# Kernel tuning notes

Hardware: AMD Instinct MI355X
Metric: run time of the kernel (lower is better)

## Reference

```python
import jax, jax.numpy as jnp
import numpy as np
import math

DIM = 1024
NUM_HEADS = 16
HEAD_DIM = DIM // NUM_HEADS
WINDOW = 256


def setup_inputs() -> dict:
    key = jax.random.key(0)
    k1, k2, k3 = jax.random.split(key, 3)
    B, T = 2, 2048
    x = jax.random.normal(k1, (B, T, DIM), dtype=jnp.float32)
    # nn.Linear weights: [out, in]; y = x @ W.T
    w_qkv = jax.random.normal(k2, (3 * DIM, DIM), dtype=jnp.float32) * (1.0 / math.sqrt(DIM))
    w_out = jax.random.normal(k3, (DIM, DIM), dtype=jnp.float32) * (1.0 / math.sqrt(DIM))
    return {"x": x, "w_qkv": w_qkv, "w_out": w_out}


def _apply_rotary(x, cos, sin):
    # x: [B,H,T,D]; cos/sin: [T, D//2] broadcast over B,H
    d = x.shape[-1] // 2
    x1, x2 = x[..., :d], x[..., d:]
    return jnp.concatenate([x1 * cos - x2 * sin, x2 * cos + x1 * sin], axis=-1)


def reference(x, w_qkv, w_out):
    B, T, C = x.shape
    H, Dh = NUM_HEADS, HEAD_DIM
    qkv = (x @ w_qkv.T).reshape(B, T, 3, H, Dh)
    q, k, v = qkv[:, :, 0], qkv[:, :, 1], qkv[:, :, 2]  # [B,T,H,Dh]
    q = jnp.transpose(q, (0, 2, 1, 3))  # [B,H,T,Dh]
    k = jnp.transpose(k, (0, 2, 1, 3))
    v = jnp.transpose(v, (0, 2, 1, 3))
    # RoPE tables
    inv_freq = 1.0 / (10000.0 ** (jnp.arange(0, Dh, 2, dtype=jnp.float32) / Dh))
    t = jnp.arange(T, dtype=jnp.float32)
    freqs = jnp.einsum('i,j->ij', t, inv_freq)  # [T, Dh//2]
    cos, sin = jnp.cos(freqs), jnp.sin(freqs)
    q = _apply_rotary(q, cos, sin)
    k = _apply_rotary(k, cos, sin)
    scale = 1.0 / math.sqrt(Dh)
    attn = jnp.einsum('bhqd,bhkd->bhqk', q, k) * scale  # [B,H,T,T]
    i = jnp.arange(T)[:, None]
    j = jnp.arange(T)[None, :]
    allowed = (j <= i) & ((i - j) < WINDOW)  # causal + sliding window
    attn = jnp.where(allowed, attn, -jnp.inf)
    attn = jax.nn.softmax(attn, axis=-1)
    out = jnp.einsum('bhqk,bhkd->bhqd', attn, v)
    out = jnp.transpose(out, (0, 2, 1, 3)).reshape(B, T, C)
    return out @ w_out.T
```

## Files before the change

kernel.cpp:

```cpp
#include <hip/hip_runtime.h>
#include <stdint.h>
#include <math.h>

#define T_SEQ 2048
#define NHEAD 16
#define WIN 256

typedef unsigned short u16;
typedef __attribute__((ext_vector_type(8))) short short8;
typedef __attribute__((ext_vector_type(4))) float f32x4;

typedef const __attribute__((address_space(1))) void* gas_ptr;
typedef __attribute__((address_space(3))) void* las_ptr;

__device__ __forceinline__ u16 f2bf(float f) {
  uint32_t u = __builtin_bit_cast(uint32_t, f);
  u += 0x7fffu + ((u >> 16) & 1u);
  return (u16)(u >> 16);
}
__device__ __forceinline__ float bf2f(u16 v) {
  return __builtin_bit_cast(float, ((uint32_t)v) << 16);
}
__device__ __forceinline__ void g2l16(const u16* g, u16* l) {
  __builtin_amdgcn_global_load_lds((gas_ptr)g, (las_ptr)l, 16, 0, 0);
}

__global__ __launch_bounds__(256) void cast_bf16_k(const float* __restrict__ in,
                                                   u16* __restrict__ out, int n4) {
  int i = blockIdx.x * 256 + threadIdx.x;
  if (i >= n4) return;
  const float4 v = reinterpret_cast<const float4*>(in)[i];
  union { u16 h[4]; uint64_t q; } o;
  o.h[0] = f2bf(v.x); o.h[1] = f2bf(v.y); o.h[2] = f2bf(v.z); o.h[3] = f2bf(v.w);
  reinterpret_cast<uint64_t*>(out)[i] = o.q;
}

template <typename OUT_T>
__global__ __launch_bounds__(256) void gemm_nt(const u16* __restrict__ A,
                                               const u16* __restrict__ B,
                                               OUT_T* __restrict__ C,
                                               int M, int N, int K) {
  __shared__ u16 lA[3][4096];
  __shared__ u16 lB[3][4096];
  const int tid = threadIdx.x;
  const int lane = tid & 63;
  const int wave = tid >> 6;
  const int r = lane & 15, g = lane >> 4;
  const int wr = wave >> 1, wc = wave & 1;

  const int nbn = N >> 7;
  const int bnpx = nbn >> 3;
  const int bid = blockIdx.x;
  const int xcd = bid & 7, ii = bid >> 3;
  const int bn = xcd * bnpx + (ii % bnpx);
  const int bm = ii / bnpx;

  const u16* Abase = A + (size_t)bm * 128 * K;
  const u16* Bbase = B + (size_t)bn * 128 * K;

  f32x4 acc[4][4];
#pragma unroll
  for (int m = 0; m < 4; m++)
#pragma unroll
    for (int n = 0; n < 4; n++) acc[m][n] = (f32x4){0.f, 0.f, 0.f, 0.f};

  const int c0 = tid, c1 = 256 + tid;
  const int row0 = c0 >> 2, row1 = c1 >> 2;
  const int sw0 = ((c0 & 3) ^ (row0 & 3)) * 8;
  const int sw1 = ((c1 & 3) ^ (row1 & 3)) * 8;
  const int ldsb = wave * 512;

  auto stage = [&](int k0, int b) {
    g2l16(Abase + (size_t)row0 * K + k0 + sw0, &lA[b][ldsb]);
    g2l16(Abase + (size_t)row1 * K + k0 + sw1, &lA[b][2048 + ldsb]);
    g2l16(Bbase + (size_t)row0 * K + k0 + sw0, &lB[b][ldsb]);
    g2l16(Bbase + (size_t)row1 * K + k0 + sw1, &lB[b][2048 + ldsb]);
  };

  const int nt = K >> 5;
  stage(0, 0);
  if (nt > 1) stage(32, 1);
  int cur = 0, pre = 2;

  const int rsw = (r & 3);
  for (int t = 0; t < nt; ++t) {
    if (t + 1 < nt) asm volatile("s_waitcnt vmcnt(4)" ::: "memory");
    else            asm volatile("s_waitcnt vmcnt(0)" ::: "memory");
    __builtin_amdgcn_s_barrier();
    if (t + 2 < nt) stage((t + 2) * 32, pre);

    const u16* la = lA[cur];
    const u16* lb = lB[cur];
    short8 af[4], bfr[4];
#pragma unroll
    for (int m = 0; m < 4; m++)
      af[m] = *reinterpret_cast<const short8*>(
          &la[(wr * 64 + m * 16 + r) * 32 + ((g ^ rsw) * 8)]);
#pragma unroll
    for (int n = 0; n < 4; n++)
      bfr[n] = *reinterpret_cast<const short8*>(
          &lb[(wc * 64 + n * 16 + r) * 32 + ((g ^ rsw) * 8)]);
#pragma unroll
    for (int m = 0; m < 4; m++)
#pragma unroll
      for (int n = 0; n < 4; n++)
        acc[m][n] = __builtin_amdgcn_mfma_f32_16x16x32_bf16(af[m], bfr[n], acc[m][n], 0, 0, 0);
    asm volatile("s_waitcnt lgkmcnt(0)" ::: "memory");
    cur = (cur == 2) ? 0 : cur + 1;
    pre = (pre == 2) ? 0 : pre + 1;
  }

#pragma unroll
  for (int m = 0; m < 4; m++) {
    const int row = bm * 128 + wr * 64 + m * 16 + g * 4;
#pragma unroll
    for (int n = 0; n < 4; n++) {
      const int col = bn * 128 + wc * 64 + n * 16 + r;
#pragma unroll
      for (int j = 0; j < 4; j++) {
        float v = acc[m][n][j];
        if constexpr (sizeof(OUT_T) == 2)
          C[(size_t)(row + j) * N + col] = f2bf(v);
        else
          C[(size_t)(row + j) * N + col] = v;
      }
    }
  }
}

__global__ __launch_bounds__(256) void rope_qk(const u16* __restrict__ qkv,
                                               u16* __restrict__ Qb,
                                               u16* __restrict__ Kb) {
  int idx = blockIdx.x * 256 + threadIdx.x;
  int d = idx & 31;
  int t = (idx >> 5) & (T_SEQ - 1);
  int h = (idx >> 16) & (NHEAD - 1);
  int b = idx >> 20;
  size_t mrow = ((size_t)(b * T_SEQ + t)) * 3072;
  int hd = h * 64 + d;
  float q1 = bf2f(qkv[mrow + hd]);
  float q2 = bf2f(qkv[mrow + hd + 32]);
  float k1 = bf2f(qkv[mrow + 1024 + hd]);
  float k2 = bf2f(qkv[mrow + 1024 + hd + 32]);
  float inv = exp2f(-(float)d * 0.41524101186092029f);
  float ang = (float)t * inv;
  float s, c;
  __sincosf(ang, &s, &c);
  size_t orow = ((size_t)((b * NHEAD + h) * T_SEQ + t)) * 64 + d;
  Qb[orow]      = f2bf(q1 * c - q2 * s);
  Qb[orow + 32] = f2bf(q2 * c + q1 * s);
  Kb[orow]      = f2bf(k1 * c - k2 * s);
  Kb[orow + 32] = f2bf(k2 * c + k1 * s);
}

__global__ __launch_bounds__(256) void v_trans(const u16* __restrict__ qkv,
                                               u16* __restrict__ Vt) {
  __shared__ u16 tile[64][72];
  const int t0 = blockIdx.x * 64;
  const int bh = blockIdx.y;
  const int b = bh >> 4, h = bh & 15;
  const int tid = threadIdx.x;
#pragma unroll
  for (int it = 0; it < 16; it++) {
    int idx = it * 256 + tid;
    int tl = idx >> 6, d = idx & 63;
    tile[tl][d] = qkv[((size_t)(b * T_SEQ + t0 + tl)) * 3072 + 2048 + h * 64 + d];
  }
  __syncthreads();
#pragma unroll
  for (int it = 0; it < 16; it++) {
    int idx = it * 256 + tid;
    int d = idx >> 6, tl = idx & 63;
    Vt[((size_t)bh * 64 + d) * T_SEQ + t0 + tl] = tile[tl][d];
  }
}

__device__ __forceinline__ void stage_kv(const u16* __restrict__ Kh,
                                         const u16* __restrict__ Vh, int k0,
                                         u16* lk, u16* lv, int tid) {
  const int wave = tid >> 6;
#pragma unroll
  for (int p = 0; p < 2; p++) {
    int c = p * 256 + tid;
    int row = c >> 3;
    int col = ((c & 7) ^ (row & 7)) * 8;
    g2l16(Kh + (size_t)(k0 + row) * 64 + col, lk + p * 2048 + wave * 512);
    g2l16(Vh + (size_t)row * T_SEQ + k0 + col, lv + p * 2048 + wave * 512);
  }
}

__global__ __launch_bounds__(256) void attn_k(const u16* __restrict__ Qb,
                                              const u16* __restrict__ Kb,
                                              const u16* __restrict__ Vt,
                                              u16* __restrict__ Ob) {
  const int bid = blockIdx.x;
  const int owned = (bid & 7) * 128 + (bid >> 3);
  const int qt = owned & 31;
  const int bh = owned >> 5;

  const int tid = threadIdx.x, lane = tid & 63, w = tid >> 6;
  const int r = lane & 15, g = lane >> 4;
  const int q0 = qt * 64;
  const u16* Qh = Qb + (size_t)bh * T_SEQ * 64;
  const u16* Kh = Kb + (size_t)bh * T_SEQ * 64;
  const u16* Vh = Vt + (size_t)bh * 64 * T_SEQ;

  __shared__ u16 lK[2][64 * 64];
  __shared__ u16 lV[2][64 * 64];
  __shared__ u16 p_lds[4][16][72];

  short8 aq[2];
#pragma unroll
  for (int kk = 0; kk < 2; kk++)
    aq[kk] = *reinterpret_cast<const short8*>(
        &Qh[(size_t)(q0 + w * 16 + r) * 64 + kk * 32 + g * 8]);

  f32x4 o[4];
#pragma unroll
  for (int n = 0; n < 4; n++) o[n] = (f32x4){0.f, 0.f, 0.f, 0.f};
  float mrun[4], lrun[4];
#pragma unroll
  for (int j = 0; j < 4; j++) { mrun[j] = -1e30f; lrun[j] = 0.f; }

  const int ktlo = (qt >= 4) ? (qt - 4) : 0;
  stage_kv(Kh, Vh, qt * 64, lK[0], lV[0], tid);
  __syncthreads();
  int buf = 0;

  for (int kt = qt; kt >= ktlo; kt--) {
    const int k0 = kt * 64;
    if (kt > ktlo)
      stage_kv(Kh, Vh, (kt - 1) * 64, lK[buf ^ 1], lV[buf ^ 1], tid);

    const u16* lk = lK[buf];
    const u16* lv = lV[buf];
    const int sw = (r & 7) * 8;

    f32x4 s[4];
#pragma unroll
    for (int n = 0; n < 4; n++) {
      f32x4 sn = (f32x4){0.f, 0.f, 0.f, 0.f};
#pragma unroll
      for (int kk = 0; kk < 2; kk++) {
        short8 bk = *reinterpret_cast<const short8*>(
            &lk[(n * 16 + r) * 64 + ((kk * 32 + g * 8) ^ sw)]);
        sn = __builtin_amdgcn_mfma_f32_16x16x32_bf16(aq[kk], bk, sn, 0, 0, 0);
      }
      s[n] = sn;
    }
    float rmax[4] = {-1e30f, -1e30f, -1e30f, -1e30f};
#pragma unroll
    for (int n = 0; n < 4; n++) {
      const int k = k0 + n * 16 + r;
#pragma unroll
      for (int j = 0; j < 4; j++) {
        const int q = q0 + w * 16 + g * 4 + j;
        float v = s[n][j] * 0.125f;
        bool ok = (k <= q) && (q - k < WIN);
        v = ok ? v : -1e30f;
        s[n][j] = v;
        rmax[j] = fmaxf(rmax[j], v);
      }
    }
#pragma unroll
    for (int off = 1; off < 16; off <<= 1)
#pragma unroll
      for (int j = 0; j < 4; j++) rmax[j] = fmaxf(rmax[j], __shfl_xor(rmax[j], off));

    float scl[4];
#pragma unroll
    for (int j = 0; j < 4; j++) {
      float mn = fmaxf(mrun[j], rmax[j]);
      scl[j] = __expf(mrun[j] - mn);
      mrun[j] = mn;
    }
    float rsum[4] = {0.f, 0.f, 0.f, 0.f};
#pragma unroll
    for (int n = 0; n < 4; n++)
#pragma unroll
      for (int j = 0; j < 4; j++) {
        float p = __expf(s[n][j] - mrun[j]);
        s[n][j] = p;
        rsum[j] += p;
      }
#pragma unroll
    for (int off = 1; off < 16; off <<= 1)
#pragma unroll
      for (int j = 0; j < 4; j++) rsum[j] += __shfl_xor(rsum[j], off);
#pragma unroll
    for (int j = 0; j < 4; j++) lrun[j] = lrun[j] * scl[j] + rsum[j];
#pragma unroll
    for (int n = 0; n < 4; n++)
#pragma unroll
      for (int j = 0; j < 4; j++) o[n][j] *= scl[j];

#pragma unroll
    for (int n = 0; n < 4; n++)
#pragma unroll
      for (int j = 0; j < 4; j++) p_lds[w][g * 4 + j][n * 16 + r] = f2bf(s[n][j]);
#pragma unroll
    for (int kk = 0; kk < 2; kk++) {
      short8 ap = *reinterpret_cast<const short8*>(&p_lds[w][r][kk * 32 + g * 8]);
#pragma unroll
      for (int n = 0; n < 4; n++) {
        short8 bv = *reinterpret_cast<const short8*>(
            &lv[(n * 16 + r) * 64 + ((kk * 32 + g * 8) ^ sw)]);
        o[n] = __builtin_amdgcn_mfma_f32_16x16x32_bf16(ap, bv, o[n], 0, 0, 0);
      }
    }
    __syncthreads();
    buf ^= 1;
  }

  const int b = bh >> 4, h = bh & 15;
#pragma unroll
  for (int n = 0; n < 4; n++)
#pragma unroll
    for (int j = 0; j < 4; j++) {
      const int q = q0 + w * 16 + g * 4 + j;
      size_t off = ((size_t)(b * T_SEQ + q)) * 1024 + h * 64 + n * 16 + r;
      Ob[off] = f2bf(o[n][j] / lrun[j]);
    }
}

extern "C" void kernel_launch(void* const* d_in, const int* in_sizes, int n_in,
                              void* d_out, int out_size, void* d_ws, size_t ws_size,
                              hipStream_t stream) {
  const float* x = (const float*)d_in[0];
  const float* w_qkv = (const float*)d_in[1];
  const float* w_out = (const float*)d_in[2];
  float* out = (float*)d_out;
  char* ws = (char*)d_ws;

  u16* xb    = (u16*)(ws + 0);
  u16* wqkvb = (u16*)(ws + 8388608);
  u16* qkvb  = (u16*)(ws + 16777216);
  u16* Qb    = (u16*)(ws + 0);
  u16* Kb    = (u16*)(ws + 8388608);
  u16* Vt    = (u16*)(ws + 41943040);
  u16* woutb = (u16*)(ws + 50331648);
  u16* Ob    = (u16*)(ws + 16777216);

  cast_bf16_k<<<4096, 256, 0, stream>>>(x, xb, 1048576);
  cast_bf16_k<<<3072, 256, 0, stream>>>(w_qkv, wqkvb, 786432);
  cast_bf16_k<<<1024, 256, 0, stream>>>(w_out, woutb, 262144);

  gemm_nt<u16><<<768, 256, 0, stream>>>(xb, wqkvb, qkvb, 4096, 3072, 1024);

  rope_qk<<<8192, 256, 0, stream>>>(qkvb, Qb, Kb);
  v_trans<<<dim3(32, 32), 256, 0, stream>>>(qkvb, Vt);

  attn_k<<<1024, 256, 0, stream>>>(Qb, Kb, Vt, Ob);

  gemm_nt<float><<<256, 256, 0, stream>>>(Ob, woutb, out, 4096, 1024, 1024);
}
```

Measured before the change: 183.7 us.

## Fuse RoPE and V transpose into the QKV GEMM epilogue

The QKV projection GEMM now writes its output directly as rotated Q and K in head-major layout and as transposed V, using each wave's accumulator tile (64 rows by one head of 64 columns). This removes the separate rope_qk and v_trans kernels and the intermediate qkv buffer round-trip through memory. In exchange, the epilogue stores are scattered 2-byte writes (V transposed with stride T_SEQ, Q/K with stride 64) and sincos is evaluated per element inside the GEMM. The workspace layout is reassigned so Q, K, V and O no longer alias the input buffers.

```diff
diff --git a/kernel.cpp b/kernel.cpp
--- a/kernel.cpp
+++ b/kernel.cpp
@@ -35,10 +35,13 @@
   reinterpret_cast<uint64_t*>(out)[i] = o.q;
 }
 
-template <typename OUT_T>
+template <int MODE, typename OUT_T>
 __global__ __launch_bounds__(256) void gemm_nt(const u16* __restrict__ A,
                                                const u16* __restrict__ B,
                                                OUT_T* __restrict__ C,
+                                               u16* __restrict__ Qb,
+                                               u16* __restrict__ Kb,
+                                               u16* __restrict__ Vt,
                                                int M, int N, int K) {
   __shared__ u16 lA[3][4096];
   __shared__ u16 lB[3][4096];
@@ -110,68 +113,64 @@
     pre = (pre == 2) ? 0 : pre + 1;
   }
 
-#pragma unroll
-  for (int m = 0; m < 4; m++) {
-    const int row = bm * 128 + wr * 64 + m * 16 + g * 4;
-#pragma unroll
-    for (int n = 0; n < 4; n++) {
-      const int col = bn * 128 + wc * 64 + n * 16 + r;
-#pragma unroll
-      for (int j = 0; j < 4; j++) {
-        float v = acc[m][n][j];
-        if constexpr (sizeof(OUT_T) == 2)
-          C[(size_t)(row + j) * N + col] = f2bf(v);
-        else
-          C[(size_t)(row + j) * N + col] = v;
-      }
-    }
-  }
-}
-
-__global__ __launch_bounds__(256) void rope_qk(const u16* __restrict__ qkv,
-                                               u16* __restrict__ Qb,
-                                               u16* __restrict__ Kb) {
-  int idx = blockIdx.x * 256 + threadIdx.x;
-  int d = idx & 31;
-  int t = (idx >> 5) & (T_SEQ - 1);
-  int h = (idx >> 16) & (NHEAD - 1);
-  int b = idx >> 20;
-  size_t mrow = ((size_t)(b * T_SEQ + t)) * 3072;
-  int hd = h * 64 + d;
-  float q1 = bf2f(qkv[mrow + hd]);
-  float q2 = bf2f(qkv[mrow + hd + 32]);
-  float k1 = bf2f(qkv[mrow + 1024 + hd]);
-  float k2 = bf2f(qkv[mrow + 1024 + hd + 32]);
-  float inv = exp2f(-(float)d * 0.41524101186092029f);
-  float ang = (float)t * inv;
-  float s, c;
-  __sincosf(ang, &s, &c);
-  size_t orow = ((size_t)((b * NHEAD + h) * T_SEQ + t)) * 64 + d;
-  Qb[orow]      = f2bf(q1 * c - q2 * s);
-  Qb[orow + 32] = f2bf(q2 * c + q1 * s);
-  Kb[orow]      = f2bf(k1 * c - k2 * s);
-  Kb[orow + 32] = f2bf(k2 * c + k1 * s);
-}
-
-__global__ __launch_bounds__(256) void v_trans(const u16* __restrict__ qkv,
-                                               u16* __restrict__ Vt) {
-  __shared__ u16 tile[64][72];
-  const int t0 = blockIdx.x * 64;
-  const int bh = blockIdx.y;
-  const int b = bh >> 4, h = bh & 15;
-  const int tid = threadIdx.x;
-#pragma unroll
-  for (int it = 0; it < 16; it++) {
-    int idx = it * 256 + tid;
-    int tl = idx >> 6, d = idx & 63;
-    tile[tl][d] = qkv[((size_t)(b * T_SEQ + t0 + tl)) * 3072 + 2048 + h * 64 + d];
-  }
-  __syncthreads();
-#pragma unroll
-  for (int it = 0; it < 16; it++) {
-    int idx = it * 256 + tid;
-    int d = idx >> 6, tl = idx & 63;
-    Vt[((size_t)bh * 64 + d) * T_SEQ + t0 + tl] = tile[tl][d];
+  if constexpr (MODE == 0) {
+#pragma unroll
+    for (int m = 0; m < 4; m++) {
+      const int row = bm * 128 + wr * 64 + m * 16 + g * 4;
+#pragma unroll
+      for (int n = 0; n < 4; n++) {
+        const int col = bn * 128 + wc * 64 + n * 16 + r;
+#pragma unroll
+        for (int j = 0; j < 4; j++) {
+          float v = acc[m][n][j];
+          if constexpr (sizeof(OUT_T) == 2)
+            C[(size_t)(row + j) * N + col] = f2bf(v);
+          else
+            C[(size_t)(row + j) * N + col] = v;
+        }
+      }
+    }
+  } else {
+    const int reg = bn >> 3;
+    const int b = bm >> 4;
+    const int h = ((bn & 7) << 1) + wc;
+    const int bh = b * NHEAD + h;
+    const int t0 = ((bm & 15) << 7) + wr * 64;
+
+    if (reg == 2) {
+      u16* vb = Vt + (size_t)bh * 64 * T_SEQ;
+#pragma unroll
+      for (int n = 0; n < 4; n++) {
+        const int d = n * 16 + r;
+#pragma unroll
+        for (int m = 0; m < 4; m++) {
+          const int t = t0 + m * 16 + g * 4;
+#pragma unroll
+          for (int j = 0; j < 4; j++)
+            vb[(size_t)d * T_SEQ + t + j] = f2bf(acc[m][n][j]);
+        }
+      }
+    } else {
+      u16* qk = (reg == 0 ? Qb : Kb) + (size_t)bh * T_SEQ * 64;
+#pragma unroll
+      for (int n = 0; n < 2; n++) {
+        const int d = n * 16 + r;
+        const float inv = exp2f(-(float)d * 0.41524101186092029f);
+#pragma unroll
+        for (int m = 0; m < 4; m++) {
+          const int tb = t0 + m * 16 + g * 4;
+#pragma unroll
+          for (int j = 0; j < 4; j++) {
+            const int t = tb + j;
+            float s, c;
+            __sincosf((float)t * inv, &s, &c);
+            const float x1 = acc[m][n][j], x2 = acc[m][n + 2][j];
+            qk[(size_t)t * 64 + d]      = f2bf(x1 * c - x2 * s);
+            qk[(size_t)t * 64 + d + 32] = f2bf(x2 * c + x1 * s);
+          }
+        }
+      }
+    }
   }
 }
 
@@ -334,23 +333,22 @@
 
   u16* xb    = (u16*)(ws + 0);
   u16* wqkvb = (u16*)(ws + 8388608);
-  u16* qkvb  = (u16*)(ws + 16777216);
-  u16* Qb    = (u16*)(ws + 0);
-  u16* Kb    = (u16*)(ws + 8388608);
-  u16* Vt    = (u16*)(ws + 41943040);
+  u16* Qb    = (u16*)(ws + 16777216);
+  u16* Kb    = (u16*)(ws + 25165824);
+  u16* Vt    = (u16*)(ws + 33554432);
+  u16* Ob    = (u16*)(ws + 41943040);
   u16* woutb = (u16*)(ws + 50331648);
-  u16* Ob    = (u16*)(ws + 16777216);
 
   cast_bf16_k<<<4096, 256, 0, stream>>>(x, xb, 1048576);
   cast_bf16_k<<<3072, 256, 0, stream>>>(w_qkv, wqkvb, 786432);
   cast_bf16_k<<<1024, 256, 0, stream>>>(w_out, woutb, 262144);
 
-  gemm_nt<u16><<<768, 256, 0, stream>>>(xb, wqkvb, qkvb, 4096, 3072, 1024);
-
-  rope_qk<<<8192, 256, 0, stream>>>(qkvb, Qb, Kb);
-  v_trans<<<dim3(32, 32), 256, 0, stream>>>(qkvb, Vt);
+  gemm_nt<1, u16><<<768, 256, 0, stream>>>(xb, wqkvb, (u16*)nullptr,
+                                           Qb, Kb, Vt, 4096, 3072, 1024);
 
   attn_k<<<1024, 256, 0, stream>>>(Qb, Kb, Vt, Ob);
 
-  gemm_nt<float><<<256, 256, 0, stream>>>(Ob, woutb, out, 4096, 1024, 1024);
-}
+  gemm_nt<0, float><<<256, 256, 0, stream>>>(Ob, woutb, out,
+                                             nullptr, nullptr, nullptr,
+                                             4096, 1024, 1024);
+}
```

New measurement: 171.9 us. -6.4%, faster.
